# Kernel optimization log

Measured on AMD Instinct MI355X. Metric: run time of the kernel, lower is better.

The kernel has to match this reference:

```python
import jax, jax.numpy as jnp
import numpy as np

N_NODES = 50000
N_EDGES = 800000
H = 128       # num_hidden
NUM_INV = 32  # num_inv


def _glorot(key, shape):
    fan_in, fan_out = shape[0], shape[1]
    lim = np.sqrt(6.0 / (fan_in + fan_out)).astype(np.float32)
    return jax.random.uniform(key, shape, jnp.float32, -lim, lim)


def setup_inputs() -> dict:
    key = jax.random.key(0)
    ks = jax.random.split(key, 12)
    x = jax.random.normal(ks[0], (N_NODES, H), jnp.float32)
    adj = jax.random.randint(ks[1], (2, N_EDGES), 0, N_NODES, dtype=jnp.int64)
    inv = jax.random.normal(ks[2], (N_EDGES, NUM_INV), jnp.float32)
    # MessageLayer: message_mlp = Linear(2H+inv -> H), SiLU, Linear(H -> H), SiLU
    Wm1 = _glorot(ks[3], (2 * H + NUM_INV, H)); bm1 = jnp.zeros((H,), jnp.float32)
    Wm2 = _glorot(ks[4], (H, H));               bm2 = jnp.zeros((H,), jnp.float32)
    # edge_inf_mlp = Linear(H -> 1), Sigmoid
    We = _glorot(ks[5], (H, 1));                be = jnp.zeros((1,), jnp.float32)
    # UpdateLayer (num_mes=1): update_mlp = Linear(2H -> H), SiLU, Linear(H -> H)
    Wu1 = _glorot(ks[6], (2 * H, H));           bu1 = jnp.zeros((H,), jnp.float32)
    Wu2 = _glorot(ks[7], (H, H));               bu2 = jnp.zeros((H,), jnp.float32)
    return {"x": x, "adj": adj, "inv": inv,
            "Wm1": Wm1, "bm1": bm1, "Wm2": Wm2, "bm2": bm2,
            "We": We, "be": be,
            "Wu1": Wu1, "bu1": bu1, "Wu2": Wu2, "bu2": bu2}


def reference(x, adj, inv, Wm1, bm1, Wm2, bm2, We, be, Wu1, bu1, Wu2, bu2):
    send, rec = adj[0], adj[1]
    # MessageLayer: gather endpoints, concat with invariants, 2-layer SiLU MLP
    state = jnp.concatenate([x[send], x[rec], inv], axis=1)      # [E, 2H+inv]
    h = jax.nn.silu(state @ Wm1 + bm1)                           # [E, H]
    msg = jax.nn.silu(h @ Wm2 + bm2)                             # [E, H]
    gate = jax.nn.sigmoid(msg @ We + be)                         # [E, 1]
    aggr = jax.ops.segment_sum(msg * gate, rec, num_segments=x.shape[0])  # [N, H]
    # UpdateLayer: concat [x, aggregated message], Linear-SiLU-Linear
    upd_in = jnp.concatenate([x, aggr], axis=1)                  # [N, 2H]
    x_up = jax.nn.silu(upd_in @ Wu1 + bu1) @ Wu2 + bu2           # [N, H]
    # Residual add
    return x + x_up
```

## Files before the change

### kernel.cpp

```cpp
#include <hip/hip_runtime.h>
#include <math.h>

#define NNODES 50000
#define NEDGES 800000
#define HDIM 128
#define NINV 32
#define K1 288
#define NTILES_E 25000
#define NTILES_N 1563
#define NB 196

#define PREP_NB 400
#define X2BF_NB 3125
#define HIST_NB 3125

#define W1STRIDE 296
#define U1STRIDE 264
#define HSTRIDE 132
#define FSTRIDE 66

typedef float floatx4 __attribute__((ext_vector_type(4)));
typedef short short8  __attribute__((ext_vector_type(8)));

union V4S8 { uint4 u; short8 s; int2 d[2]; };

__device__ __forceinline__ float silu_f(float z) { return z / (1.0f + __expf(-z)); }

__device__ __forceinline__ unsigned short f2bf_rne(float f) {
    unsigned u = __float_as_uint(f);
    u += 0x7fffu + ((u >> 16) & 1u);
    return (unsigned short)(u >> 16);
}

__device__ __forceinline__ unsigned pk_bf(float hi, float lo) {
    return __builtin_amdgcn_perm(__float_as_uint(hi), __float_as_uint(lo), 0x07060302);
}

__device__ __forceinline__ short8 cvt8(float4 f0, float4 f1) {
    V4S8 v;
    v.u.x = pk_bf(f0.y, f0.x);
    v.u.y = pk_bf(f0.w, f0.z);
    v.u.z = pk_bf(f1.y, f1.x);
    v.u.w = pk_bf(f1.w, f1.z);
    return v.s;
}

__device__ __forceinline__ int adj_at(const void* adj, int is64, long long pos) {
    if (is64) return (int)((const long long*)adj)[pos];
    return ((const int*)adj)[pos];
}

__device__ __forceinline__ int detect64(const int* __restrict__ adj32) {
    int l = threadIdx.x & 63;
    int v = adj32[2 * l + 1] | adj32[2 * (l + 64) + 1]
          | adj32[2 * (l + 128) + 1] | adj32[2 * (l + 192) + 1];
    return (__ballot(v != 0) == 0ull) ? 1 : 0;
}

__global__ __launch_bounds__(256) void prep_all(
    const float* __restrict__ Wm1, const float* __restrict__ Wm2,
    const float* __restrict__ Wu1, const float* __restrict__ Wu2,
    unsigned short* __restrict__ Wm1t, unsigned short* __restrict__ Wm2t,
    unsigned short* __restrict__ Wu1t, unsigned short* __restrict__ Wu2t,
    const float* __restrict__ x, unsigned short* __restrict__ xbf,
    const void* __restrict__ adj, int* __restrict__ hist)
{
    int bid = blockIdx.x;
    if (bid < PREP_NB) {
        int i = bid * 256 + threadIdx.x;
        if (i < 128 * K1) {
            int n = i / K1, k = i % K1;
            Wm1t[i] = f2bf_rne(Wm1[k * HDIM + n]);
        } else if ((i -= 128 * K1) < 128 * HDIM) {
            int n = i / HDIM, k = i % HDIM;
            Wm2t[i] = f2bf_rne(Wm2[k * HDIM + n]);
        } else if ((i -= 128 * HDIM) < 128 * 256) {
            int n = i / 256, k = i % 256;
            Wu1t[i] = f2bf_rne(Wu1[k * HDIM + n]);
        } else if ((i -= 128 * 256) < 128 * HDIM) {
            int n = i / HDIM, k = i % HDIM;
            Wu2t[i] = f2bf_rne(Wu2[k * HDIM + n]);
        }
    } else if (bid < PREP_NB + X2BF_NB) {
        int i = (bid - PREP_NB) * 256 + threadIdx.x;
        if (i < NNODES * HDIM / 8) {
            const float4* p = (const float4*)(x + i * 8);
            float4 f0 = p[0], f1 = p[1];
            uint4 u;
            u.x = pk_bf(f0.y, f0.x);
            u.y = pk_bf(f0.w, f0.z);
            u.z = pk_bf(f1.y, f1.x);
            u.w = pk_bf(f1.w, f1.z);
            unsigned short s0 = f2bf_rne(f0.x), s1 = f2bf_rne(f0.y), s2 = f2bf_rne(f0.z), s3 = f2bf_rne(f0.w);
            unsigned short s4 = f2bf_rne(f1.x), s5 = f2bf_rne(f1.y), s6 = f2bf_rne(f1.z), s7 = f2bf_rne(f1.w);
            u.x = (unsigned)s0 | ((unsigned)s1 << 16);
            u.y = (unsigned)s2 | ((unsigned)s3 << 16);
            u.z = (unsigned)s4 | ((unsigned)s5 << 16);
            u.w = (unsigned)s6 | ((unsigned)s7 << 16);
            *(uint4*)(xbf + i * 8) = u;
        }
    } else {
        int is64 = detect64((const int*)adj);
        int e = (bid - PREP_NB - X2BF_NB) * 256 + threadIdx.x;
        if (e < NEDGES) {
            int r = adj_at(adj, is64, (long long)NEDGES + e);
            atomicAdd(&hist[r], 1);
        }
    }
}

__global__ __launch_bounds__(256) void scanA_kernel(const int* __restrict__ hist,
                                                    int* __restrict__ bsum)
{
    __shared__ int red[256];
    int i = blockIdx.x * 256 + threadIdx.x;
    int v = (i < NNODES) ? hist[i] : 0;
    red[threadIdx.x] = v;
    __syncthreads();
    for (int d = 128; d > 0; d >>= 1) {
        if (threadIdx.x < d) red[threadIdx.x] += red[threadIdx.x + d];
        __syncthreads();
    }
    if (threadIdx.x == 0) bsum[blockIdx.x] = red[0];
}

__global__ __launch_bounds__(256) void scanC_kernel(const int* __restrict__ hist,
                                                    const int* __restrict__ bsum,
                                                    int* __restrict__ cursor)
{
    __shared__ int sb[256];
    __shared__ int s[256];
    int t = threadIdx.x;
    sb[t] = (t < NB) ? bsum[t] : 0;
    int i = blockIdx.x * 256 + t;
    int v = (i < NNODES) ? hist[i] : 0;
    s[t] = v;
    __syncthreads();
    for (int d = 1; d < 256; d <<= 1) {
        int ub = (t >= d) ? sb[t - d] : 0;
        int us = (t >= d) ? s[t - d] : 0;
        __syncthreads();
        sb[t] += ub;
        s[t]  += us;
        __syncthreads();
    }
    int boff = (blockIdx.x == 0) ? 0 : sb[blockIdx.x - 1];
    if (i < NNODES) cursor[i] = boff + s[t] - v;
}

__global__ __launch_bounds__(256) void scatter_kernel(const void* __restrict__ adj,
                                                      int* __restrict__ cursor,
                                                      int4* __restrict__ sEdge)
{
    int is64 = detect64((const int*)adj);
    int e = blockIdx.x * 256 + threadIdx.x;
    if (e < NEDGES) {
        int s = adj_at(adj, is64, e);
        int r = adj_at(adj, is64, (long long)NEDGES + e);
        int pos = atomicAdd(&cursor[r], 1);
        sEdge[pos] = make_int4(s, r, e, 0);
    }
}

__global__ __launch_bounds__(512, 2) void edge_kernel(
    const unsigned short* __restrict__ xbf, const float* __restrict__ inv,
    const int4* __restrict__ sEdge,
    const unsigned short* __restrict__ Wm1t, const float* __restrict__ bm1,
    const unsigned short* __restrict__ Wm2t, const float* __restrict__ bm2,
    const float* __restrict__ We, const float* __restrict__ be,
    float* __restrict__ aggr)
{
    __shared__ unsigned short s_w1[128 * W1STRIDE];
    __shared__ unsigned short s_h[8 * 32 * HSTRIDE];
    __shared__ int s_recb[8 * 32];

    const int t    = threadIdx.x;
    const int l    = t & 63;
    const int wid  = t >> 6;
    const int l15  = l & 15;
    const int quad = l >> 4;

    for (int idx = t; idx < 128 * 36; idx += 512) {
        int n = idx / 36, c = idx % 36;
        *(uint4*)&s_w1[n * W1STRIDE + c * 8] = *(const uint4*)(Wm1t + n * K1 + c * 8);
    }

    short8 w2f[4][8];
    #pragma unroll
    for (int ks = 0; ks < 4; ++ks)
        #pragma unroll
        for (int nt = 0; nt < 8; ++nt)
            w2f[ks][nt] = *(const short8*)(Wm2t + (nt * 16 + l15) * HDIM + ks * 32 + quad * 8);

    float bm1v[8], bm2v[8], wev[8];
    #pragma unroll
    for (int nt = 0; nt < 8; ++nt) {
        bm1v[nt] = bm1[nt * 16 + l15];
        bm2v[nt] = bm2[nt * 16 + l15];
        wev[nt]  = We[nt * 16 + l15];
    }
    const float be0 = be[0];

    __syncthreads();

    unsigned short* hbuf = s_h + wid * (32 * HSTRIDE);
    int* srec = s_recb + wid * 32;
    const int gwave  = blockIdx.x * 8 + wid;
    const int nwaves = gridDim.x * 8;
    const int t_lo = (int)((long long)gwave * NTILES_E / nwaves);
    const int t_hi = (int)((long long)(gwave + 1) * NTILES_E / nwaves);
    if (t_lo >= t_hi) return;

    int4 iA = sEdge[t_lo * 32 + l15];
    int4 iB = sEdge[t_lo * 32 + 16 + l15];
    unsigned oS0 = (unsigned)iA.x * HDIM, oR0 = (unsigned)iA.y * HDIM, oI0 = (unsigned)iA.z * NINV;
    unsigned oS1 = (unsigned)iB.x * HDIM, oR1 = (unsigned)iB.y * HDIM, oI1 = (unsigned)iB.z * NINV;

    short8 F[8][2];
    #pragma unroll
    for (int s = 0; s < 4; ++s) {
        F[s][0] = *(const short8*)(xbf + oS0 + s * 32 + quad * 8);
        F[s][1] = *(const short8*)(xbf + oS1 + s * 32 + quad * 8);
    }

    for (int tile = t_lo; tile < t_hi; ++tile) {
        const bool nv = (tile + 1) < t_hi;
        int4 nA, nB;
        if (nv) {
            nA = sEdge[(tile + 1) * 32 + l15];
            nB = sEdge[(tile + 1) * 32 + 16 + l15];
        }
        const int re0 = iA.y, re1 = iB.y;

        #pragma unroll
        for (int s = 0; s < 4; ++s) {
            F[4 + s][0] = *(const short8*)(xbf + oR0 + s * 32 + quad * 8);
            F[4 + s][1] = *(const short8*)(xbf + oR1 + s * 32 + quad * 8);
        }
        float4 I0[2], I1[2];
        {
            const float* p0 = inv + oI0 + quad * 8;
            const float* p1 = inv + oI1 + quad * 8;
            I0[0] = ((const float4*)p0)[0]; I0[1] = ((const float4*)p0)[1];
            I1[0] = ((const float4*)p1)[0]; I1[1] = ((const float4*)p1)[1];
        }

        floatx4 acc[2][8];
        #pragma unroll
        for (int nt = 0; nt < 8; ++nt) {
            acc[0][nt] = (floatx4){bm1v[nt], bm1v[nt], bm1v[nt], bm1v[nt]};
            acc[1][nt] = acc[0][nt];
        }

        short8 Fi0, Fi1;
        #pragma unroll
        for (int s = 0; s < 9; ++s) {
            short8 a0, a1;
            if (s < 8) { a0 = F[s][0]; a1 = F[s][1]; }
            else       { a0 = Fi0;     a1 = Fi1;     }
            if (s == 6) {
                Fi0 = cvt8(I0[0], I0[1]);
                Fi1 = cvt8(I1[0], I1[1]);
            }
            const unsigned short* wbase = s_w1 + l15 * W1STRIDE + s * 32 + quad * 8;
            #pragma unroll
            for (int nt = 0; nt < 8; ++nt) {
                short8 b = *(const short8*)(wbase + nt * 16 * W1STRIDE);
                acc[0][nt] = __builtin_amdgcn_mfma_f32_16x16x32_bf16(a0, b, acc[0][nt], 0, 0, 0);
                acc[1][nt] = __builtin_amdgcn_mfma_f32_16x16x32_bf16(a1, b, acc[1][nt], 0, 0, 0);
            }
        }

        #pragma unroll
        for (int m = 0; m < 2; ++m)
            #pragma unroll
            for (int nt = 0; nt < 8; ++nt)
                #pragma unroll
                for (int r = 0; r < 4; ++r) {
                    float hv = silu_f(acc[m][nt][r]);
                    hbuf[(m * 16 + quad * 4 + r) * HSTRIDE + nt * 16 + l15] =
                        (unsigned short)(__float_as_uint(hv) >> 16);
                }

        #pragma unroll
        for (int nt = 0; nt < 8; ++nt) {
            acc[0][nt] = (floatx4){bm2v[nt], bm2v[nt], bm2v[nt], bm2v[nt]};
            acc[1][nt] = acc[0][nt];
        }

        #pragma unroll
        for (int ks = 0; ks < 4; ++ks) {
            short8 a2[2];
            #pragma unroll
            for (int m = 0; m < 2; ++m) {
                int base = (m * 16 + l15) * HSTRIDE + ks * 32 + quad * 8;
                V4S8 v;
                v.d[0] = *(const int2*)(hbuf + base);
                v.d[1] = *(const int2*)(hbuf + base + 4);
                a2[m] = v.s;
            }
            #pragma unroll
            for (int nt = 0; nt < 8; ++nt) {
                acc[0][nt] = __builtin_amdgcn_mfma_f32_16x16x32_bf16(a2[0], w2f[ks][nt], acc[0][nt], 0, 0, 0);
                acc[1][nt] = __builtin_amdgcn_mfma_f32_16x16x32_bf16(a2[1], w2f[ks][nt], acc[1][nt], 0, 0, 0);
            }
        }

        if (nv) {
            iA = nA; iB = nB;
            oS0 = (unsigned)iA.x * HDIM; oR0 = (unsigned)iA.y * HDIM; oI0 = (unsigned)iA.z * NINV;
            oS1 = (unsigned)iB.x * HDIM; oR1 = (unsigned)iB.y * HDIM; oI1 = (unsigned)iB.z * NINV;
            #pragma unroll
            for (int s = 0; s < 4; ++s) {
                F[s][0] = *(const short8*)(xbf + oS0 + s * 32 + quad * 8);
                F[s][1] = *(const short8*)(xbf + oS1 + s * 32 + quad * 8);
            }
        }

        #pragma unroll
        for (int m = 0; m < 2; ++m)
            #pragma unroll
            for (int nt = 0; nt < 8; ++nt)
                #pragma unroll
                for (int r = 0; r < 4; ++r)
                    acc[m][nt][r] = silu_f(acc[m][nt][r]);

        float g[2][4];
        #pragma unroll
        for (int m = 0; m < 2; ++m)
            #pragma unroll
            for (int r = 0; r < 4; ++r) {
                float part = 0.f;
                #pragma unroll
                for (int nt = 0; nt < 8; ++nt)
                    part = fmaf(acc[m][nt][r], wev[nt], part);
                part += __shfl_xor(part, 1);
                part += __shfl_xor(part, 2);
                part += __shfl_xor(part, 4);
                part += __shfl_xor(part, 8);
                g[m][r] = 1.0f / (1.0f + __expf(-(part + be0)));
            }

        if (quad == 0) { srec[l15] = re0; srec[16 + l15] = re1; }

        float* fred = (float*)hbuf;
        #pragma unroll
        for (int half = 0; half < 2; ++half) {
            #pragma unroll
            for (int m = 0; m < 2; ++m)
                #pragma unroll
                for (int nt2 = 0; nt2 < 4; ++nt2)
                    #pragma unroll
                    for (int r = 0; r < 4; ++r)
                        fred[(m * 16 + quad * 4 + r) * FSTRIDE + nt2 * 16 + l15] =
                            acc[m][half * 4 + nt2][r] * g[m][r];

            float* dstbase = aggr + half * 64 + l;
            float sum = 0.f;
            int prev = srec[0];
            #pragma unroll
            for (int row = 0; row < 32; ++row) {
                float v = fred[row * FSTRIDE + l];
                int rc = srec[row];
                if (rc != prev) {
                    atomicAdd(dstbase + (unsigned)prev * HDIM, sum);
                    sum = 0.f;
                    prev = rc;
                }
                sum += v;
            }
            atomicAdd(dstbase + (unsigned)prev * HDIM, sum);
        }
    }
}

__global__ __launch_bounds__(256) void node_kernel(
    const float* __restrict__ x, const unsigned short* __restrict__ xbf,
    const float* __restrict__ aggr,
    const unsigned short* __restrict__ Wu1t, const float* __restrict__ bu1,
    const unsigned short* __restrict__ Wu2t, const float* __restrict__ bu2,
    float* __restrict__ out)
{
    __shared__ unsigned short s_u1[128 * U1STRIDE];
    __shared__ unsigned short s_h[4 * 32 * HSTRIDE];

    const int t    = threadIdx.x;
    const int l    = t & 63;
    const int wid  = t >> 6;
    const int l15  = l & 15;
    const int quad = l >> 4;

    for (int idx = t; idx < 128 * 32; idx += 256) {
        int n = idx / 32, c = idx % 32;
        *(uint4*)&s_u1[n * U1STRIDE + c * 8] = *(const uint4*)(Wu1t + n * 256 + c * 8);
    }

    short8 w2f[4][8];
    #pragma unroll
    for (int ks = 0; ks < 4; ++ks)
        #pragma unroll
        for (int nt = 0; nt < 8; ++nt)
            w2f[ks][nt] = *(const short8*)(Wu2t + (nt * 16 + l15) * HDIM + ks * 32 + quad * 8);

    float bu1v[8], bu2v[8];
    #pragma unroll
    for (int nt = 0; nt < 8; ++nt) {
        bu1v[nt] = bu1[nt * 16 + l15];
        bu2v[nt] = bu2[nt * 16 + l15];
    }

    __syncthreads();

    unsigned short* hbuf = s_h + wid * (32 * HSTRIDE);
    const int nwaves = gridDim.x * 4;

    for (int tile = blockIdx.x * 4 + wid; tile < NTILES_N; tile += nwaves) {
        const int n0 = tile * 32;

        unsigned offX[2];
        #pragma unroll
        for (int m = 0; m < 2; ++m) {
            int row = n0 + m * 16 + l15;
            if (row >= NNODES) row = NNODES - 1;
            offX[m] = (unsigned)row * HDIM;
        }

        floatx4 acc[2][8];
        #pragma unroll
        for (int nt = 0; nt < 8; ++nt) {
            acc[0][nt] = (floatx4){bu1v[nt], bu1v[nt], bu1v[nt], bu1v[nt]};
            acc[1][nt] = acc[0][nt];
        }

        #pragma unroll
        for (int s = 0; s < 8; ++s) {
            short8 a[2];
            #pragma unroll
            for (int m = 0; m < 2; ++m) {
                if (s < 4) {
                    a[m] = *(const short8*)(xbf + offX[m] + s * 32 + quad * 8);
                } else {
                    const float* p = aggr + offX[m] + (s - 4) * 32 + quad * 8;
                    a[m] = cvt8(((const float4*)p)[0], ((const float4*)p)[1]);
                }
            }
            const unsigned short* wbase = s_u1 + l15 * U1STRIDE + s * 32 + quad * 8;
            #pragma unroll
            for (int nt = 0; nt < 8; ++nt) {
                short8 b = *(const short8*)(wbase + nt * 16 * U1STRIDE);
                acc[0][nt] = __builtin_amdgcn_mfma_f32_16x16x32_bf16(a[0], b, acc[0][nt], 0, 0, 0);
                acc[1][nt] = __builtin_amdgcn_mfma_f32_16x16x32_bf16(a[1], b, acc[1][nt], 0, 0, 0);
            }
        }

        #pragma unroll
        for (int m = 0; m < 2; ++m)
            #pragma unroll
            for (int nt = 0; nt < 8; ++nt)
                #pragma unroll
                for (int r = 0; r < 4; ++r) {
                    float hv = silu_f(acc[m][nt][r]);
                    hbuf[(m * 16 + quad * 4 + r) * HSTRIDE + nt * 16 + l15] =
                        (unsigned short)(__float_as_uint(hv) >> 16);
                }

        #pragma unroll
        for (int nt = 0; nt < 8; ++nt) {
            acc[0][nt] = (floatx4){bu2v[nt], bu2v[nt], bu2v[nt], bu2v[nt]};
            acc[1][nt] = acc[0][nt];
        }

        #pragma unroll
        for (int ks = 0; ks < 4; ++ks) {
            short8 a2[2];
            #pragma unroll
            for (int m = 0; m < 2; ++m) {
                int base = (m * 16 + l15) * HSTRIDE + ks * 32 + quad * 8;
                V4S8 v;
                v.d[0] = *(const int2*)(hbuf + base);
                v.d[1] = *(const int2*)(hbuf + base + 4);
                a2[m] = v.s;
            }
            #pragma unroll
            for (int nt = 0; nt < 8; ++nt) {
                acc[0][nt] = __builtin_amdgcn_mfma_f32_16x16x32_bf16(a2[0], w2f[ks][nt], acc[0][nt], 0, 0, 0);
                acc[1][nt] = __builtin_amdgcn_mfma_f32_16x16x32_bf16(a2[1], w2f[ks][nt], acc[1][nt], 0, 0, 0);
            }
        }

        #pragma unroll
        for (int m = 0; m < 2; ++m)
            #pragma unroll
            for (int r = 0; r < 4; ++r) {
                int row = n0 + m * 16 + quad * 4 + r;
                if (row < NNODES) {
                    #pragma unroll
                    for (int nt = 0; nt < 8; ++nt) {
                        int col = nt * 16 + l15;
                        out[(long long)row * HDIM + col] = x[(long long)row * HDIM + col] + acc[m][nt][r];
                    }
                }
            }
    }
}

extern "C" void kernel_launch(void* const* d_in, const int* in_sizes, int n_in,
                              void* d_out, int out_size, void* d_ws, size_t ws_size,
                              hipStream_t stream)
{
    const float* x   = (const float*)d_in[0];
    const void*  adj = d_in[1];
    const float* inv = (const float*)d_in[2];
    const float* Wm1 = (const float*)d_in[3];
    const float* bm1 = (const float*)d_in[4];
    const float* Wm2 = (const float*)d_in[5];
    const float* bm2 = (const float*)d_in[6];
    const float* We  = (const float*)d_in[7];
    const float* be  = (const float*)d_in[8];
    const float* Wu1 = (const float*)d_in[9];
    const float* bu1 = (const float*)d_in[10];
    const float* Wu2 = (const float*)d_in[11];
    const float* bu2 = (const float*)d_in[12];
    float* out = (float*)d_out;

    char* ws = (char*)d_ws;
    float* aggr = (float*)ws;
    size_t off = (size_t)NNODES * HDIM * 4;
    int* hist   = (int*)(ws + off);          off += (size_t)NNODES * 4;
    unsigned short* Wm1t = (unsigned short*)(ws + off);  off += 128 * K1 * 2;
    unsigned short* Wm2t = (unsigned short*)(ws + off);  off += 128 * HDIM * 2;
    unsigned short* Wu1t = (unsigned short*)(ws + off);  off += 128 * 256 * 2;
    unsigned short* Wu2t = (unsigned short*)(ws + off);  off += 128 * HDIM * 2;
    off = (off + 63) & ~(size_t)63;
    unsigned short* xbf = (unsigned short*)(ws + off);   off += (size_t)NNODES * HDIM * 2;
    int* cursor = (int*)(ws + off);          off += (size_t)NNODES * 4;
    int* bsum   = (int*)(ws + off);          off += 1024;
    off = (off + 63) & ~(size_t)63;
    int4* sEdge = (int4*)(ws + off);         off += (size_t)NEDGES * 16;

    hipMemsetAsync(aggr, 0, (size_t)(NNODES * HDIM + NNODES) * sizeof(float), stream);
    prep_all<<<PREP_NB + X2BF_NB + HIST_NB, 256, 0, stream>>>(
        Wm1, Wm2, Wu1, Wu2, Wm1t, Wm2t, Wu1t, Wu2t, x, xbf, adj, hist);
    scanA_kernel<<<NB, 256, 0, stream>>>(hist, bsum);
    scanC_kernel<<<NB, 256, 0, stream>>>(hist, bsum, cursor);
    scatter_kernel<<<(NEDGES + 255) / 256, 256, 0, stream>>>(adj, cursor, sEdge);
    edge_kernel<<<256, 512, 0, stream>>>(xbf, inv, sEdge,
                                         Wm1t, bm1, Wm2t, bm2, We, be, aggr);
    node_kernel<<<256, 256, 0, stream>>>(x, xbf, aggr, Wu1t, bu1, Wu2t, bu2, out);
}
```

Measured before the change: 609.1 us.

## Stream MLP weights from global/L2 instead of LDS and registers to raise occupancy

Removes the per-block LDS staging of the first-layer weights and the register-resident second-layer weight fragments in both the edge and node kernels. Weight B-operands are now loaded directly from global memory, relying on L1/L2 caching, inside the MFMA loops. This frees LDS and VGPRs so launch bounds can allow 4 blocks per CU, and the grids grow to 512 blocks and one wave per node tile. The trade-off is many more global and L2 weight loads in the inner loop, which may stall the MFMA pipeline. It also deletes a dead pk_bf packing sequence in the x-to-bf16 conversion.

```diff
diff --git a/kernel.cpp b/kernel.cpp
--- a/kernel.cpp
+++ b/kernel.cpp
@@ -14,8 +14,6 @@
 #define X2BF_NB 3125
 #define HIST_NB 3125
 
-#define W1STRIDE 296
-#define U1STRIDE 264
 #define HSTRIDE 132
 #define FSTRIDE 66
 
@@ -86,13 +84,9 @@
         if (i < NNODES * HDIM / 8) {
             const float4* p = (const float4*)(x + i * 8);
             float4 f0 = p[0], f1 = p[1];
-            uint4 u;
-            u.x = pk_bf(f0.y, f0.x);
-            u.y = pk_bf(f0.w, f0.z);
-            u.z = pk_bf(f1.y, f1.x);
-            u.w = pk_bf(f1.w, f1.z);
             unsigned short s0 = f2bf_rne(f0.x), s1 = f2bf_rne(f0.y), s2 = f2bf_rne(f0.z), s3 = f2bf_rne(f0.w);
             unsigned short s4 = f2bf_rne(f1.x), s5 = f2bf_rne(f1.y), s6 = f2bf_rne(f1.z), s7 = f2bf_rne(f1.w);
+            uint4 u;
             u.x = (unsigned)s0 | ((unsigned)s1 << 16);
             u.y = (unsigned)s2 | ((unsigned)s3 << 16);
             u.z = (unsigned)s4 | ((unsigned)s5 << 16);
@@ -162,7 +156,7 @@
     }
 }
 
-__global__ __launch_bounds__(512, 2) void edge_kernel(
+__global__ __launch_bounds__(512, 4) void edge_kernel(
     const unsigned short* __restrict__ xbf, const float* __restrict__ inv,
     const int4* __restrict__ sEdge,
     const unsigned short* __restrict__ Wm1t, const float* __restrict__ bm1,
@@ -170,7 +164,6 @@
     const float* __restrict__ We, const float* __restrict__ be,
     float* __restrict__ aggr)
 {
-    __shared__ unsigned short s_w1[128 * W1STRIDE];
     __shared__ unsigned short s_h[8 * 32 * HSTRIDE];
     __shared__ int s_recb[8 * 32];
 
@@ -179,18 +172,6 @@
     const int wid  = t >> 6;
     const int l15  = l & 15;
     const int quad = l >> 4;
-
-    for (int idx = t; idx < 128 * 36; idx += 512) {
-        int n = idx / 36, c = idx % 36;
-        *(uint4*)&s_w1[n * W1STRIDE + c * 8] = *(const uint4*)(Wm1t + n * K1 + c * 8);
-    }
-
-    short8 w2f[4][8];
-    #pragma unroll
-    for (int ks = 0; ks < 4; ++ks)
-        #pragma unroll
-        for (int nt = 0; nt < 8; ++nt)
-            w2f[ks][nt] = *(const short8*)(Wm2t + (nt * 16 + l15) * HDIM + ks * 32 + quad * 8);
 
     float bm1v[8], bm2v[8], wev[8];
     #pragma unroll
@@ -201,7 +182,8 @@
     }
     const float be0 = be[0];
 
-    __syncthreads();
+    const unsigned short* w1base = Wm1t + (unsigned)l15 * K1 + quad * 8;
+    const unsigned short* w2base = Wm2t + (unsigned)l15 * HDIM + quad * 8;
 
     unsigned short* hbuf = s_h + wid * (32 * HSTRIDE);
     int* srec = s_recb + wid * 32;
@@ -262,10 +244,10 @@
                 Fi0 = cvt8(I0[0], I0[1]);
                 Fi1 = cvt8(I1[0], I1[1]);
             }
-            const unsigned short* wbase = s_w1 + l15 * W1STRIDE + s * 32 + quad * 8;
+            const unsigned short* wb = w1base + s * 32;
             #pragma unroll
             for (int nt = 0; nt < 8; ++nt) {
-                short8 b = *(const short8*)(wbase + nt * 16 * W1STRIDE);
+                short8 b = *(const short8*)(wb + nt * 16 * K1);
                 acc[0][nt] = __builtin_amdgcn_mfma_f32_16x16x32_bf16(a0, b, acc[0][nt], 0, 0, 0);
                 acc[1][nt] = __builtin_amdgcn_mfma_f32_16x16x32_bf16(a1, b, acc[1][nt], 0, 0, 0);
             }
@@ -299,10 +281,12 @@
                 v.d[1] = *(const int2*)(hbuf + base + 4);
                 a2[m] = v.s;
             }
+            const unsigned short* wb2 = w2base + ks * 32;
             #pragma unroll
             for (int nt = 0; nt < 8; ++nt) {
-                acc[0][nt] = __builtin_amdgcn_mfma_f32_16x16x32_bf16(a2[0], w2f[ks][nt], acc[0][nt], 0, 0, 0);
-                acc[1][nt] = __builtin_amdgcn_mfma_f32_16x16x32_bf16(a2[1], w2f[ks][nt], acc[1][nt], 0, 0, 0);
+                short8 b = *(const short8*)(wb2 + nt * 16 * HDIM);
+                acc[0][nt] = __builtin_amdgcn_mfma_f32_16x16x32_bf16(a2[0], b, acc[0][nt], 0, 0, 0);
+                acc[1][nt] = __builtin_amdgcn_mfma_f32_16x16x32_bf16(a2[1], b, acc[1][nt], 0, 0, 0);
             }
         }
 
@@ -374,14 +358,13 @@
     }
 }
 
-__global__ __launch_bounds__(256) void node_kernel(
+__global__ __launch_bounds__(256, 4) void node_kernel(
     const float* __restrict__ x, const unsigned short* __restrict__ xbf,
     const float* __restrict__ aggr,
     const unsigned short* __restrict__ Wu1t, const float* __restrict__ bu1,
     const unsigned short* __restrict__ Wu2t, const float* __restrict__ bu2,
     float* __restrict__ out)
 {
-    __shared__ unsigned short s_u1[128 * U1STRIDE];
     __shared__ unsigned short s_h[4 * 32 * HSTRIDE];
 
     const int t    = threadIdx.x;
@@ -390,18 +373,6 @@
     const int l15  = l & 15;
     const int quad = l >> 4;
 
-    for (int idx = t; idx < 128 * 32; idx += 256) {
-        int n = idx / 32, c = idx % 32;
-        *(uint4*)&s_u1[n * U1STRIDE + c * 8] = *(const uint4*)(Wu1t + n * 256 + c * 8);
-    }
-
-    short8 w2f[4][8];
-    #pragma unroll
-    for (int ks = 0; ks < 4; ++ks)
-        #pragma unroll
-        for (int nt = 0; nt < 8; ++nt)
-            w2f[ks][nt] = *(const short8*)(Wu2t + (nt * 16 + l15) * HDIM + ks * 32 + quad * 8);
-
     float bu1v[8], bu2v[8];
     #pragma unroll
     for (int nt = 0; nt < 8; ++nt) {
@@ -409,7 +380,8 @@
         bu2v[nt] = bu2[nt * 16 + l15];
     }
 
-    __syncthreads();
+    const unsigned short* u1base = Wu1t + (unsigned)l15 * 256 + quad * 8;
+    const unsigned short* u2base = Wu2t + (unsigned)l15 * HDIM + quad * 8;
 
     unsigned short* hbuf = s_h + wid * (32 * HSTRIDE);
     const int nwaves = gridDim.x * 4;
@@ -444,10 +416,10 @@
                     a[m] = cvt8(((const float4*)p)[0], ((const float4*)p)[1]);
                 }
             }
-            const unsigned short* wbase = s_u1 + l15 * U1STRIDE + s * 32 + quad * 8;
+            const unsigned short* wb = u1base + s * 32;
             #pragma unroll
             for (int nt = 0; nt < 8; ++nt) {
-                short8 b = *(const short8*)(wbase + nt * 16 * U1STRIDE);
+                short8 b = *(const short8*)(wb + nt * 16 * 256);
                 acc[0][nt] = __builtin_amdgcn_mfma_f32_16x16x32_bf16(a[0], b, acc[0][nt], 0, 0, 0);
                 acc[1][nt] = __builtin_amdgcn_mfma_f32_16x16x32_bf16(a[1], b, acc[1][nt], 0, 0, 0);
             }
@@ -481,10 +453,12 @@
                 v.d[1] = *(const int2*)(hbuf + base + 4);
                 a2[m] = v.s;
             }
+            const unsigned short* wb2 = u2base + ks * 32;
             #pragma unroll
             for (int nt = 0; nt < 8; ++nt) {
-                acc[0][nt] = __builtin_amdgcn_mfma_f32_16x16x32_bf16(a2[0], w2f[ks][nt], acc[0][nt], 0, 0, 0);
-                acc[1][nt] = __builtin_amdgcn_mfma_f32_16x16x32_bf16(a2[1], w2f[ks][nt], acc[1][nt], 0, 0, 0);
+                short8 b = *(const short8*)(wb2 + nt * 16 * HDIM);
+                acc[0][nt] = __builtin_amdgcn_mfma_f32_16x16x32_bf16(a2[0], b, acc[0][nt], 0, 0, 0);
+                acc[1][nt] = __builtin_amdgcn_mfma_f32_16x16x32_bf16(a2[1], b, acc[1][nt], 0, 0, 0);
             }
         }
 
@@ -544,7 +518,8 @@
     scanA_kernel<<<NB, 256, 0, stream>>>(hist, bsum);
     scanC_kernel<<<NB, 256, 0, stream>>>(hist, bsum, cursor);
     scatter_kernel<<<(NEDGES + 255) / 256, 256, 0, stream>>>(adj, cursor, sEdge);
-    edge_kernel<<<256, 512, 0, stream>>>(xbf, inv, sEdge,
+    edge_kernel<<<512, 512, 0, stream>>>(xbf, inv, sEdge,
                                          Wm1t, bm1, Wm2t, bm2, We, be, aggr);
-    node_kernel<<<256, 256, 0, stream>>>(x, xbf, aggr, Wu1t, bu1, Wu2t, bu2, out);
-}
+    node_kernel<<<(NTILES_N + 3) / 4, 256, 0, stream>>>(x, xbf, aggr,
+                                                        Wu1t, bu1, Wu2t, bu2, out);
+}
```

After: 1.773 ms. 191% more time.

## Use 1024-thread edge blocks with halved hbuf and register-based segmented reduction

Applied to the files above, without the earlier changes.

The edge kernel now runs 16 waves per block instead of 8 by shrinking each wave's hidden-activation scratch to 16 rows and processing the two 16-row MFMA halves of the second GEMM one after another. The gated reduction by receiver no longer stages floats through shared memory. It finds segment boundaries with a ballot, sums rows in registers with cross-quad shuffles, and issues one atomic per segment per column. The next tile's gather is moved later so it overlaps the reduction. The node kernel moves to 512-thread blocks with a grid sized to the tile count. Risks are register pressure under the 1024-thread launch bound and a serial segment loop when receiver ids are highly fragmented.

```diff
diff --git a/kernel.cpp b/kernel.cpp
--- a/kernel.cpp
+++ b/kernel.cpp
@@ -17,7 +17,6 @@
 #define W1STRIDE 296
 #define U1STRIDE 264
 #define HSTRIDE 132
-#define FSTRIDE 66
 
 typedef float floatx4 __attribute__((ext_vector_type(4)));
 typedef short short8  __attribute__((ext_vector_type(8)));
@@ -86,13 +85,9 @@
         if (i < NNODES * HDIM / 8) {
             const float4* p = (const float4*)(x + i * 8);
             float4 f0 = p[0], f1 = p[1];
-            uint4 u;
-            u.x = pk_bf(f0.y, f0.x);
-            u.y = pk_bf(f0.w, f0.z);
-            u.z = pk_bf(f1.y, f1.x);
-            u.w = pk_bf(f1.w, f1.z);
             unsigned short s0 = f2bf_rne(f0.x), s1 = f2bf_rne(f0.y), s2 = f2bf_rne(f0.z), s3 = f2bf_rne(f0.w);
             unsigned short s4 = f2bf_rne(f1.x), s5 = f2bf_rne(f1.y), s6 = f2bf_rne(f1.z), s7 = f2bf_rne(f1.w);
+            uint4 u;
             u.x = (unsigned)s0 | ((unsigned)s1 << 16);
             u.y = (unsigned)s2 | ((unsigned)s3 << 16);
             u.z = (unsigned)s4 | ((unsigned)s5 << 16);
@@ -162,7 +157,7 @@
     }
 }
 
-__global__ __launch_bounds__(512, 2) void edge_kernel(
+__global__ __launch_bounds__(1024, 1) void edge_kernel(
     const unsigned short* __restrict__ xbf, const float* __restrict__ inv,
     const int4* __restrict__ sEdge,
     const unsigned short* __restrict__ Wm1t, const float* __restrict__ bm1,
@@ -171,8 +166,8 @@
     float* __restrict__ aggr)
 {
     __shared__ unsigned short s_w1[128 * W1STRIDE];
-    __shared__ unsigned short s_h[8 * 32 * HSTRIDE];
-    __shared__ int s_recb[8 * 32];
+    __shared__ unsigned short s_h[16 * 16 * HSTRIDE];
+    __shared__ int s_recb[16 * 32];
 
     const int t    = threadIdx.x;
     const int l    = t & 63;
@@ -180,7 +175,7 @@
     const int l15  = l & 15;
     const int quad = l >> 4;
 
-    for (int idx = t; idx < 128 * 36; idx += 512) {
+    for (int idx = t; idx < 128 * 36; idx += 1024) {
         int n = idx / 36, c = idx % 36;
         *(uint4*)&s_w1[n * W1STRIDE + c * 8] = *(const uint4*)(Wm1t + n * K1 + c * 8);
     }
@@ -203,10 +198,10 @@
 
     __syncthreads();
 
-    unsigned short* hbuf = s_h + wid * (32 * HSTRIDE);
+    unsigned short* hbuf = s_h + wid * (16 * HSTRIDE);
     int* srec = s_recb + wid * 32;
-    const int gwave  = blockIdx.x * 8 + wid;
-    const int nwaves = gridDim.x * 8;
+    const int gwave  = blockIdx.x * 16 + wid;
+    const int nwaves = gridDim.x * 16;
     const int t_lo = (int)((long long)gwave * NTILES_E / nwaves);
     const int t_hi = (int)((long long)(gwave + 1) * NTILES_E / nwaves);
     if (t_lo >= t_hi) return;
@@ -272,49 +267,49 @@
         }
 
         #pragma unroll
-        for (int m = 0; m < 2; ++m)
+        for (int nt = 0; nt < 8; ++nt)
+            #pragma unroll
+            for (int r = 0; r < 4; ++r) {
+                float hv = silu_f(acc[0][nt][r]);
+                hbuf[(quad * 4 + r) * HSTRIDE + nt * 16 + l15] =
+                    (unsigned short)(__float_as_uint(hv) >> 16);
+            }
+        #pragma unroll
+        for (int nt = 0; nt < 8; ++nt)
+            acc[0][nt] = (floatx4){bm2v[nt], bm2v[nt], bm2v[nt], bm2v[nt]};
+        #pragma unroll
+        for (int ks = 0; ks < 4; ++ks) {
+            int base = l15 * HSTRIDE + ks * 32 + quad * 8;
+            V4S8 v;
+            v.d[0] = *(const int2*)(hbuf + base);
+            v.d[1] = *(const int2*)(hbuf + base + 4);
+            short8 a2 = v.s;
             #pragma unroll
             for (int nt = 0; nt < 8; ++nt)
-                #pragma unroll
-                for (int r = 0; r < 4; ++r) {
-                    float hv = silu_f(acc[m][nt][r]);
-                    hbuf[(m * 16 + quad * 4 + r) * HSTRIDE + nt * 16 + l15] =
-                        (unsigned short)(__float_as_uint(hv) >> 16);
-                }
-
-        #pragma unroll
-        for (int nt = 0; nt < 8; ++nt) {
-            acc[0][nt] = (floatx4){bm2v[nt], bm2v[nt], bm2v[nt], bm2v[nt]};
-            acc[1][nt] = acc[0][nt];
-        }
-
+                acc[0][nt] = __builtin_amdgcn_mfma_f32_16x16x32_bf16(a2, w2f[ks][nt], acc[0][nt], 0, 0, 0);
+        }
+
+        #pragma unroll
+        for (int nt = 0; nt < 8; ++nt)
+            #pragma unroll
+            for (int r = 0; r < 4; ++r) {
+                float hv = silu_f(acc[1][nt][r]);
+                hbuf[(quad * 4 + r) * HSTRIDE + nt * 16 + l15] =
+                    (unsigned short)(__float_as_uint(hv) >> 16);
+            }
+        #pragma unroll
+        for (int nt = 0; nt < 8; ++nt)
+            acc[1][nt] = (floatx4){bm2v[nt], bm2v[nt], bm2v[nt], bm2v[nt]};
         #pragma unroll
         for (int ks = 0; ks < 4; ++ks) {
-            short8 a2[2];
-            #pragma unroll
-            for (int m = 0; m < 2; ++m) {
-                int base = (m * 16 + l15) * HSTRIDE + ks * 32 + quad * 8;
-                V4S8 v;
-                v.d[0] = *(const int2*)(hbuf + base);
-                v.d[1] = *(const int2*)(hbuf + base + 4);
-                a2[m] = v.s;
-            }
-            #pragma unroll
-            for (int nt = 0; nt < 8; ++nt) {
-                acc[0][nt] = __builtin_amdgcn_mfma_f32_16x16x32_bf16(a2[0], w2f[ks][nt], acc[0][nt], 0, 0, 0);
-                acc[1][nt] = __builtin_amdgcn_mfma_f32_16x16x32_bf16(a2[1], w2f[ks][nt], acc[1][nt], 0, 0, 0);
-            }
-        }
-
-        if (nv) {
-            iA = nA; iB = nB;
-            oS0 = (unsigned)iA.x * HDIM; oR0 = (unsigned)iA.y * HDIM; oI0 = (unsigned)iA.z * NINV;
-            oS1 = (unsigned)iB.x * HDIM; oR1 = (unsigned)iB.y * HDIM; oI1 = (unsigned)iB.z * NINV;
-            #pragma unroll
-            for (int s = 0; s < 4; ++s) {
-                F[s][0] = *(const short8*)(xbf + oS0 + s * 32 + quad * 8);
-                F[s][1] = *(const short8*)(xbf + oS1 + s * 32 + quad * 8);
-            }
+            int base = l15 * HSTRIDE + ks * 32 + quad * 8;
+            V4S8 v;
+            v.d[0] = *(const int2*)(hbuf + base);
+            v.d[1] = *(const int2*)(hbuf + base + 4);
+            short8 a2 = v.s;
+            #pragma unroll
+            for (int nt = 0; nt < 8; ++nt)
+                acc[1][nt] = __builtin_amdgcn_mfma_f32_16x16x32_bf16(a2, w2f[ks][nt], acc[1][nt], 0, 0, 0);
         }
 
         #pragma unroll
@@ -341,40 +336,70 @@
                 g[m][r] = 1.0f / (1.0f + __expf(-(part + be0)));
             }
 
+        #pragma unroll
+        for (int m = 0; m < 2; ++m)
+            #pragma unroll
+            for (int nt = 0; nt < 8; ++nt)
+                #pragma unroll
+                for (int r = 0; r < 4; ++r)
+                    acc[m][nt][r] *= g[m][r];
+
         if (quad == 0) { srec[l15] = re0; srec[16 + l15] = re1; }
 
-        float* fred = (float*)hbuf;
-        #pragma unroll
-        for (int half = 0; half < 2; ++half) {
+        if (nv) {
+            iA = nA; iB = nB;
+            oS0 = (unsigned)iA.x * HDIM; oR0 = (unsigned)iA.y * HDIM; oI0 = (unsigned)iA.z * NINV;
+            oS1 = (unsigned)iB.x * HDIM; oR1 = (unsigned)iB.y * HDIM; oI1 = (unsigned)iB.z * NINV;
+            #pragma unroll
+            for (int s = 0; s < 4; ++s) {
+                F[s][0] = *(const short8*)(xbf + oS0 + s * 32 + quad * 8);
+                F[s][1] = *(const short8*)(xbf + oS1 + s * 32 + quad * 8);
+            }
+        }
+
+        int myrow = l & 31;
+        int rc_a = srec[myrow];
+        int rc_b = srec[(myrow > 0) ? (myrow - 1) : 0];
+        unsigned long long bmask = __ballot((l < 32) && (myrow > 0) && (rc_a != rc_b));
+
+        int lo = 0;
+        for (;;) {
+            unsigned long long rest = bmask & (~0ull << (lo + 1));
+            int hi = rest ? (__ffsll((long long)rest) - 1) : 32;
+
+            float part[8];
+            #pragma unroll
+            for (int nt = 0; nt < 8; ++nt) part[nt] = 0.f;
             #pragma unroll
             for (int m = 0; m < 2; ++m)
                 #pragma unroll
-                for (int nt2 = 0; nt2 < 4; ++nt2)
-                    #pragma unroll
-                    for (int r = 0; r < 4; ++r)
-                        fred[(m * 16 + quad * 4 + r) * FSTRIDE + nt2 * 16 + l15] =
-                            acc[m][half * 4 + nt2][r] * g[m][r];
-
-            float* dstbase = aggr + half * 64 + l;
-            float sum = 0.f;
-            int prev = srec[0];
-            #pragma unroll
-            for (int row = 0; row < 32; ++row) {
-                float v = fred[row * FSTRIDE + l];
-                int rc = srec[row];
-                if (rc != prev) {
-                    atomicAdd(dstbase + (unsigned)prev * HDIM, sum);
-                    sum = 0.f;
-                    prev = rc;
+                for (int r = 0; r < 4; ++r) {
+                    int R = m * 16 + quad * 4 + r;
+                    if (R >= lo && R < hi) {
+                        #pragma unroll
+                        for (int nt = 0; nt < 8; ++nt)
+                            part[nt] += acc[m][nt][r];
+                    }
                 }
-                sum += v;
-            }
-            atomicAdd(dstbase + (unsigned)prev * HDIM, sum);
-        }
-    }
-}
-
-__global__ __launch_bounds__(256) void node_kernel(
+            #pragma unroll
+            for (int nt = 0; nt < 8; ++nt) {
+                part[nt] += __shfl_xor(part[nt], 16);
+                part[nt] += __shfl_xor(part[nt], 32);
+            }
+            int dest = srec[lo];
+            if (quad == 0) {
+                float* dst = aggr + (unsigned)dest * HDIM + l15;
+                #pragma unroll
+                for (int nt = 0; nt < 8; ++nt)
+                    atomicAdd(dst + nt * 16, part[nt]);
+            }
+            if (hi >= 32) break;
+            lo = hi;
+        }
+    }
+}
+
+__global__ __launch_bounds__(512) void node_kernel(
     const float* __restrict__ x, const unsigned short* __restrict__ xbf,
     const float* __restrict__ aggr,
     const unsigned short* __restrict__ Wu1t, const float* __restrict__ bu1,
@@ -382,7 +407,7 @@
     float* __restrict__ out)
 {
     __shared__ unsigned short s_u1[128 * U1STRIDE];
-    __shared__ unsigned short s_h[4 * 32 * HSTRIDE];
+    __shared__ unsigned short s_h[8 * 32 * HSTRIDE];
 
     const int t    = threadIdx.x;
     const int l    = t & 63;
@@ -390,7 +415,7 @@
     const int l15  = l & 15;
     const int quad = l >> 4;
 
-    for (int idx = t; idx < 128 * 32; idx += 256) {
+    for (int idx = t; idx < 128 * 32; idx += 512) {
         int n = idx / 32, c = idx % 32;
         *(uint4*)&s_u1[n * U1STRIDE + c * 8] = *(const uint4*)(Wu1t + n * 256 + c * 8);
     }
@@ -412,9 +437,9 @@
     __syncthreads();
 
     unsigned short* hbuf = s_h + wid * (32 * HSTRIDE);
-    const int nwaves = gridDim.x * 4;
-
-    for (int tile = blockIdx.x * 4 + wid; tile < NTILES_N; tile += nwaves) {
+    const int nwaves = gridDim.x * 8;
+
+    for (int tile = blockIdx.x * 8 + wid; tile < NTILES_N; tile += nwaves) {
         const int n0 = tile * 32;
 
         unsigned offX[2];
@@ -544,7 +569,8 @@
     scanA_kernel<<<NB, 256, 0, stream>>>(hist, bsum);
     scanC_kernel<<<NB, 256, 0, stream>>>(hist, bsum, cursor);
     scatter_kernel<<<(NEDGES + 255) / 256, 256, 0, stream>>>(adj, cursor, sEdge);
-    edge_kernel<<<256, 512, 0, stream>>>(xbf, inv, sEdge,
-                                         Wm1t, bm1, Wm2t, bm2, We, be, aggr);
-    node_kernel<<<256, 256, 0, stream>>>(x, xbf, aggr, Wu1t, bu1, Wu2t, bu2, out);
-}
+    edge_kernel<<<256, 1024, 0, stream>>>(xbf, inv, sEdge,
+                                          Wm1t, bm1, Wm2t, bm2, We, be, aggr);
+    node_kernel<<<(NTILES_N + 7) / 8, 512, 0, stream>>>(x, xbf, aggr,
+                                                        Wu1t, bu1, Wu2t, bu2, out);
+}
```

Result: slower. 1.065 ms (+74.8%).
